# Optimization experiments

Measured on AMD Instinct MI355X. Metric: run time of the kernel, lower is better.

## Reference

```python
import jax, jax.numpy as jnp
import numpy as np

N = 50000
E = 800000
F_IN = 128
DIM = 256
NUM_CLASSES = 10
NUM_GRAPHS = 256


def setup_inputs() -> dict:
    key = jax.random.key(0)
    ks = jax.random.split(key, 20)
    x = jax.random.normal(ks[0], (N, F_IN), dtype=jnp.float32)
    edge_index = jax.random.randint(ks[1], (2, E), 0, N, dtype=jnp.int32)
    batch = jnp.sort(jax.random.randint(ks[2], (N,), 0, NUM_GRAPHS, dtype=jnp.int32))
    edge_weight = jnp.ones((E,), dtype=jnp.float32)

    def lin(k, fan_in, fan_out, bias=True):
        bound = 1.0 / np.sqrt(fan_in)
        k1, k2 = jax.random.split(k)
        W = jax.random.uniform(k1, (fan_in, fan_out), minval=-bound, maxval=bound, dtype=jnp.float32)
        if bias:
            b = jax.random.uniform(k2, (fan_out,), minval=-bound, maxval=bound, dtype=jnp.float32)
            return W, b
        return W

    params = {}
    dims = [(F_IN, DIM)] + [(DIM, DIM)] * 4
    for i, (fi, fo) in enumerate(dims, start=1):
        Wr, br = lin(ks[2 + 3 * i], fi, fo, bias=True)
        Wroot = lin(ks[3 + 3 * i], fi, fo, bias=False)
        params[f"W{i}_rel"] = Wr
        params[f"b{i}_rel"] = br
        params[f"W{i}_root"] = Wroot
    Wfc1, bfc1 = lin(ks[18], DIM, DIM)
    Wfc2, bfc2 = lin(ks[19], DIM, NUM_CLASSES)
    return dict(x=x, edge_index=edge_index, batch=batch, edge_weight=edge_weight,
                **params, Wfc1=Wfc1, bfc1=bfc1, Wfc2=Wfc2, bfc2=bfc2)


def graph_conv(x, src, dst, ew, W_rel, b_rel, W_root):
    # message: x_j * edge_weight, aggregated by sum at destination nodes
    msg = x[src] * ew[:, None]                                  # [E, F]
    agg = jax.ops.segment_sum(msg, dst, num_segments=N)          # [N, F]
    return agg @ W_rel + b_rel + x @ W_root


def reference(x, edge_index, batch, edge_weight,
              W1_rel, b1_rel, W1_root, W2_rel, b2_rel, W2_root,
              W3_rel, b3_rel, W3_root, W4_rel, b4_rel, W4_root,
              W5_rel, b5_rel, W5_root, Wfc1, bfc1, Wfc2, bfc2):
    src, dst = edge_index[0], edge_index[1]
    layers = [(W1_rel, b1_rel, W1_root), (W2_rel, b2_rel, W2_root),
              (W3_rel, b3_rel, W3_root), (W4_rel, b4_rel, W4_root),
              (W5_rel, b5_rel, W5_root)]
    h = x
    for Wr, br, Wroot in layers:
        h = jax.nn.relu(graph_conv(h, src, dst, edge_weight, Wr, br, Wroot))
    pooled = jax.ops.segment_sum(h, batch, num_segments=NUM_GRAPHS)  # [G, DIM]
    h = jax.nn.relu(pooled @ Wfc1 + bfc1)
    # dropout is identity in eval mode
    logits = h @ Wfc2 + bfc2
    return jax.nn.log_softmax(logits, axis=-1)
```

## Files before the change

### kernel.cpp

```cpp
#include <hip/hip_runtime.h>
#include <hip/hip_bf16.h>

#define N_NODES 50000
#define N_EDGES 800000
#define F_IN 128
#define DIM 256
#define NUM_CLASSES 10
#define NUM_GRAPHS 256
#define NBKT ((N_NODES + 255) / 256)
#define BCAP 8192
#define NRT ((N_NODES + 127) / 128)

typedef short bf16x8 __attribute__((ext_vector_type(8)));
typedef float f32x4 __attribute__((ext_vector_type(4)));

__device__ __forceinline__ float bf2f(unsigned short u) {
    union { unsigned int u; float f; } c;
    c.u = ((unsigned int)u) << 16;
    return c.f;
}
__device__ __forceinline__ unsigned short f2bf(float f) {
    union { float f; unsigned int u; } c;
    c.f = f;
    unsigned int r = (c.u + 0x7fffu + ((c.u >> 16) & 1u)) >> 16;
    return (unsigned short)r;
}
__device__ __forceinline__ float u2f(unsigned int u) {
    union { unsigned int u; float f; } c;
    c.u = u;
    return c.f;
}
__device__ __forceinline__ unsigned int f2u(float f) {
    union { float f; unsigned int u; } c;
    c.f = f;
    return c.u;
}

__device__ __forceinline__ void gload16(const unsigned short* g, unsigned short* l) {
    __builtin_amdgcn_global_load_lds(
        (const __attribute__((address_space(1))) unsigned int*)(g),
        (__attribute__((address_space(3))) unsigned int*)(l), 16, 0, 0);
}


__global__ void bucket_hist(const int* __restrict__ dst, int* __restrict__ bcnt, int E) {
    __shared__ int c[NBKT];
    int t = threadIdx.x;
    for (int i = t; i < NBKT; i += 256) c[i] = 0;
    __syncthreads();
    int ebase = blockIdx.x * 4096 + t;
#pragma unroll
    for (int i = 0; i < 16; ++i) {
        int e = ebase + i * 256;
        if (e < E) atomicAdd(&c[dst[e] >> 8], 1);
    }
    __syncthreads();
    for (int i = t; i < NBKT; i += 256)
        if (c[i]) atomicAdd(&bcnt[i], c[i]);
}

__global__ void scan_bkt(const int* __restrict__ bcnt, int* __restrict__ bbase,
                         int* __restrict__ gbase) {
    __shared__ int sd[256];
    int t = threadIdx.x;
    int v = (t < NBKT) ? bcnt[t] : 0;
    sd[t] = v;
    __syncthreads();
    for (int off = 1; off < 256; off <<= 1) {
        int u = (t >= off) ? sd[t - off] : 0;
        __syncthreads();
        sd[t] += u;
        __syncthreads();
    }
    if (t < NBKT) {
        int ex = sd[t] - v;
        bbase[t] = ex;
        gbase[t] = ex;
    }
    if (t == NBKT - 1) bbase[NBKT] = sd[t];
}

__global__ __launch_bounds__(256) void bucket_scatter(
    const int* __restrict__ src, const int* __restrict__ dst, const float* __restrict__ ew,
    int* __restrict__ gbase, uint2* __restrict__ edata2, int E) {
    __shared__ int cnt[NBKT];
    __shared__ int base_s[NBKT];
    int t = threadIdx.x;
    int ebase = blockIdx.x * 4096 + t;
    for (int i = t; i < NBKT; i += 256) cnt[i] = 0;
    __syncthreads();
#pragma unroll
    for (int i = 0; i < 16; ++i) {
        int e = ebase + i * 256;
        if (e < E) atomicAdd(&cnt[dst[e] >> 8], 1);
    }
    __syncthreads();
    for (int i = t; i < NBKT; i += 256) {
        int c = cnt[i];
        base_s[i] = c ? atomicAdd(&gbase[i], c) : 0;
        cnt[i] = 0;
    }
    __syncthreads();
#pragma unroll
    for (int i = 0; i < 16; ++i) {
        int e = ebase + i * 256;
        if (e < E) {
            int d = dst[e];
            int bkt = d >> 8;
            int r = atomicAdd(&cnt[bkt], 1);
            edata2[base_s[bkt] + r] =
                make_uint2((unsigned)src[e] | ((unsigned)(d & 255) << 16), f2u(ew[e]));
        }
    }
}

__global__ __launch_bounds__(256) void bucket_sort(
    const int* __restrict__ bbase, const uint2* __restrict__ edata2, uint2* __restrict__ edata,
    int* __restrict__ offs) {
    __shared__ uint2 stage[BCAP];
    __shared__ int cnt[256];
    __shared__ int sd[256];
    int b = blockIdx.x, t = threadIdx.x;
    int lo = bbase[b];
    int hi = bbase[b + 1];
    int ce = hi - lo;
    cnt[t] = 0;
    __syncthreads();
    for (int i = t; i < ce; i += 256) {
        uint2 e = edata2[lo + i];
        atomicAdd(&cnt[(e.x >> 16) & 255], 1);
    }
    __syncthreads();
    int myc = cnt[t];
    sd[t] = myc;
    __syncthreads();
    for (int off = 1; off < 256; off <<= 1) {
        int u = (t >= off) ? sd[t - off] : 0;
        __syncthreads();
        sd[t] += u;
        __syncthreads();
    }
    int ex = sd[t] - myc;
    __syncthreads();
    sd[t] = ex;
    cnt[t] = 0;
    int node = b * 256 + t;
    if (node < N_NODES) offs[node] = lo + ex;
    if (node == N_NODES - 1) offs[N_NODES] = lo + ex + myc;
    __syncthreads();
    if (ce <= BCAP) {
        for (int i = t; i < ce; i += 256) {
            uint2 e = edata2[lo + i];
            int dl = (e.x >> 16) & 255;
            int r = atomicAdd(&cnt[dl], 1);
            stage[sd[dl] + r] = make_uint2(e.x & 0xFFFFu, e.y);
        }
        __syncthreads();
        for (int i = t; i < ce; i += 256) edata[lo + i] = stage[i];
    } else {
        for (int i = t; i < ce; i += 256) {
            uint2 e = edata2[lo + i];
            int dl = (e.x >> 16) & 255;
            int r = atomicAdd(&cnt[dl], 1);
            edata[lo + sd[dl] + r] = make_uint2(e.x & 0xFFFFu, e.y);
        }
    }
}


__global__ void conv_x(const float* __restrict__ x, unsigned short* __restrict__ xb, int n4) {
    int i = blockIdx.x * blockDim.x + threadIdx.x;
    if (i >= n4) return;
    float4 v = ((const float4*)x)[i];
    ushort4 o;
    o.x = f2bf(v.x); o.y = f2bf(v.y); o.z = f2bf(v.z); o.w = f2bf(v.w);
    ((ushort4*)xb)[i] = o;
}

__global__ void pack_w(const float* __restrict__ Wr, const float* __restrict__ Wo,
                       unsigned short* __restrict__ Bt, int K) {
    int idx = blockIdx.x * blockDim.x + threadIdx.x;
    int total = 2 * K * DIM;
    if (idx >= total) return;
    int k = idx / DIM, c = idx % DIM;
    float v = (k < K) ? Wr[k * DIM + c] : Wo[(k - K) * DIM + c];
    Bt[(size_t)c * (2 * K) + k] = f2bf(v);
}

__global__ void pack_w4(const float* __restrict__ W2r, const float* __restrict__ W2o,
                        const float* __restrict__ W3r, const float* __restrict__ W3o,
                        const float* __restrict__ W4r, const float* __restrict__ W4o,
                        const float* __restrict__ W5r, const float* __restrict__ W5o,
                        unsigned short* __restrict__ B2, unsigned short* __restrict__ B3,
                        unsigned short* __restrict__ B4, unsigned short* __restrict__ B5) {
    int idx = blockIdx.x * blockDim.x + threadIdx.x;
    int total = 2 * DIM * DIM;
    if (idx >= total) return;
    int L = blockIdx.y;
    const float* Wr = (L == 0) ? W2r : (L == 1) ? W3r : (L == 2) ? W4r : W5r;
    const float* Wo = (L == 0) ? W2o : (L == 1) ? W3o : (L == 2) ? W4o : W5o;
    unsigned short* Bt = (L == 0) ? B2 : (L == 1) ? B3 : (L == 2) ? B4 : B5;
    int k = idx / DIM, c = idx % DIM;
    float v = (k < DIM) ? Wr[k * DIM + c] : Wo[(k - DIM) * DIM + c];
    Bt[(size_t)c * (2 * DIM) + k] = f2bf(v);
}


template <int F>
__global__ void agg_bf16(const unsigned short* __restrict__ hsrc, const int* __restrict__ offs,
                         const uint2* __restrict__ edata, unsigned short* __restrict__ agg) {
    int node = blockIdx.x * (blockDim.x >> 6) + (threadIdx.x >> 6);
    if (node >= N_NODES) return;
    int lane = threadIdx.x & 63;
    int hf = lane >> 5;
    int sl = lane & 31;
    int s0 = offs[node], s1 = offs[node + 1];
    if (F == 256) {
        const unsigned short* hb = hsrc + sl * 8;
        float acc[8] = {0.f, 0.f, 0.f, 0.f, 0.f, 0.f, 0.f, 0.f};
        int p = s0;
        for (; p + 7 < s1; p += 8) {
            uint2 e0 = edata[p + hf];
            uint2 e1 = edata[p + 2 + hf];
            uint2 e2 = edata[p + 4 + hf];
            uint2 e3 = edata[p + 6 + hf];
            float w0 = u2f(e0.y), w1 = u2f(e1.y), w2 = u2f(e2.y), w3 = u2f(e3.y);
            uint4 r0 = *(const uint4*)(hb + (size_t)e0.x * 256);
            uint4 r1 = *(const uint4*)(hb + (size_t)e1.x * 256);
            uint4 r2 = *(const uint4*)(hb + (size_t)e2.x * 256);
            uint4 r3 = *(const uint4*)(hb + (size_t)e3.x * 256);
            acc[0] += w0 * bf2f((unsigned short)r0.x);
            acc[1] += w0 * bf2f((unsigned short)(r0.x >> 16));
            acc[2] += w0 * bf2f((unsigned short)r0.y);
            acc[3] += w0 * bf2f((unsigned short)(r0.y >> 16));
            acc[4] += w0 * bf2f((unsigned short)r0.z);
            acc[5] += w0 * bf2f((unsigned short)(r0.z >> 16));
            acc[6] += w0 * bf2f((unsigned short)r0.w);
            acc[7] += w0 * bf2f((unsigned short)(r0.w >> 16));
            acc[0] += w1 * bf2f((unsigned short)r1.x);
            acc[1] += w1 * bf2f((unsigned short)(r1.x >> 16));
            acc[2] += w1 * bf2f((unsigned short)r1.y);
            acc[3] += w1 * bf2f((unsigned short)(r1.y >> 16));
            acc[4] += w1 * bf2f((unsigned short)r1.z);
            acc[5] += w1 * bf2f((unsigned short)(r1.z >> 16));
            acc[6] += w1 * bf2f((unsigned short)r1.w);
            acc[7] += w1 * bf2f((unsigned short)(r1.w >> 16));
            acc[0] += w2 * bf2f((unsigned short)r2.x);
            acc[1] += w2 * bf2f((unsigned short)(r2.x >> 16));
            acc[2] += w2 * bf2f((unsigned short)r2.y);
            acc[3] += w2 * bf2f((unsigned short)(r2.y >> 16));
            acc[4] += w2 * bf2f((unsigned short)r2.z);
            acc[5] += w2 * bf2f((unsigned short)(r2.z >> 16));
            acc[6] += w2 * bf2f((unsigned short)r2.w);
            acc[7] += w2 * bf2f((unsigned short)(r2.w >> 16));
            acc[0] += w3 * bf2f((unsigned short)r3.x);
            acc[1] += w3 * bf2f((unsigned short)(r3.x >> 16));
            acc[2] += w3 * bf2f((unsigned short)r3.y);
            acc[3] += w3 * bf2f((unsigned short)(r3.y >> 16));
            acc[4] += w3 * bf2f((unsigned short)r3.z);
            acc[5] += w3 * bf2f((unsigned short)(r3.z >> 16));
            acc[6] += w3 * bf2f((unsigned short)r3.w);
            acc[7] += w3 * bf2f((unsigned short)(r3.w >> 16));
        }
        for (; p + 3 < s1; p += 4) {
            uint2 e0 = edata[p + hf];
            uint2 e1 = edata[p + 2 + hf];
            float w0 = u2f(e0.y), w1 = u2f(e1.y);
            uint4 r0 = *(const uint4*)(hb + (size_t)e0.x * 256);
            uint4 r1 = *(const uint4*)(hb + (size_t)e1.x * 256);
            acc[0] += w0 * bf2f((unsigned short)r0.x);
            acc[1] += w0 * bf2f((unsigned short)(r0.x >> 16));
            acc[2] += w0 * bf2f((unsigned short)r0.y);
            acc[3] += w0 * bf2f((unsigned short)(r0.y >> 16));
            acc[4] += w0 * bf2f((unsigned short)r0.z);
            acc[5] += w0 * bf2f((unsigned short)(r0.z >> 16));
            acc[6] += w0 * bf2f((unsigned short)r0.w);
            acc[7] += w0 * bf2f((unsigned short)(r0.w >> 16));
            acc[0] += w1 * bf2f((unsigned short)r1.x);
            acc[1] += w1 * bf2f((unsigned short)(r1.x >> 16));
            acc[2] += w1 * bf2f((unsigned short)r1.y);
            acc[3] += w1 * bf2f((unsigned short)(r1.y >> 16));
            acc[4] += w1 * bf2f((unsigned short)r1.z);
            acc[5] += w1 * bf2f((unsigned short)(r1.z >> 16));
            acc[6] += w1 * bf2f((unsigned short)r1.w);
            acc[7] += w1 * bf2f((unsigned short)(r1.w >> 16));
        }
        for (; p < s1; p += 2) {
            int pe = p + hf;
            bool v = pe < s1;
            uint2 e = edata[v ? pe : (s1 - 1)];
            float w = v ? u2f(e.y) : 0.f;
            uint4 r = *(const uint4*)(hb + (size_t)e.x * 256);
            acc[0] += w * bf2f((unsigned short)r.x);
            acc[1] += w * bf2f((unsigned short)(r.x >> 16));
            acc[2] += w * bf2f((unsigned short)r.y);
            acc[3] += w * bf2f((unsigned short)(r.y >> 16));
            acc[4] += w * bf2f((unsigned short)r.z);
            acc[5] += w * bf2f((unsigned short)(r.z >> 16));
            acc[6] += w * bf2f((unsigned short)r.w);
            acc[7] += w * bf2f((unsigned short)(r.w >> 16));
        }
#pragma unroll
        for (int i = 0; i < 8; ++i) acc[i] += __shfl_xor(acc[i], 32, 64);
        if (hf == 0) {
            uint4 o;
            o.x = (unsigned)f2bf(acc[0]) | ((unsigned)f2bf(acc[1]) << 16);
            o.y = (unsigned)f2bf(acc[2]) | ((unsigned)f2bf(acc[3]) << 16);
            o.z = (unsigned)f2bf(acc[4]) | ((unsigned)f2bf(acc[5]) << 16);
            o.w = (unsigned)f2bf(acc[6]) | ((unsigned)f2bf(acc[7]) << 16);
            *(uint4*)(agg + (size_t)node * 256 + sl * 8) = o;
        }
    } else {
        const unsigned short* hb = hsrc + sl * 4;
        float acc[4] = {0.f, 0.f, 0.f, 0.f};
        int p = s0;
        for (; p + 7 < s1; p += 8) {
            uint2 e0 = edata[p + hf];
            uint2 e1 = edata[p + 2 + hf];
            uint2 e2 = edata[p + 4 + hf];
            uint2 e3 = edata[p + 6 + hf];
            float w0 = u2f(e0.y), w1 = u2f(e1.y), w2 = u2f(e2.y), w3 = u2f(e3.y);
            uint2 r0 = *(const uint2*)(hb + (size_t)e0.x * 128);
            uint2 r1 = *(const uint2*)(hb + (size_t)e1.x * 128);
            uint2 r2 = *(const uint2*)(hb + (size_t)e2.x * 128);
            uint2 r3 = *(const uint2*)(hb + (size_t)e3.x * 128);
            acc[0] += w0 * bf2f((unsigned short)r0.x);
            acc[1] += w0 * bf2f((unsigned short)(r0.x >> 16));
            acc[2] += w0 * bf2f((unsigned short)r0.y);
            acc[3] += w0 * bf2f((unsigned short)(r0.y >> 16));
            acc[0] += w1 * bf2f((unsigned short)r1.x);
            acc[1] += w1 * bf2f((unsigned short)(r1.x >> 16));
            acc[2] += w1 * bf2f((unsigned short)r1.y);
            acc[3] += w1 * bf2f((unsigned short)(r1.y >> 16));
            acc[0] += w2 * bf2f((unsigned short)r2.x);
            acc[1] += w2 * bf2f((unsigned short)(r2.x >> 16));
            acc[2] += w2 * bf2f((unsigned short)r2.y);
            acc[3] += w2 * bf2f((unsigned short)(r2.y >> 16));
            acc[0] += w3 * bf2f((unsigned short)r3.x);
            acc[1] += w3 * bf2f((unsigned short)(r3.x >> 16));
            acc[2] += w3 * bf2f((unsigned short)r3.y);
            acc[3] += w3 * bf2f((unsigned short)(r3.y >> 16));
        }
        for (; p + 3 < s1; p += 4) {
            uint2 e0 = edata[p + hf];
            uint2 e1 = edata[p + 2 + hf];
            float w0 = u2f(e0.y), w1 = u2f(e1.y);
            uint2 r0 = *(const uint2*)(hb + (size_t)e0.x * 128);
            uint2 r1 = *(const uint2*)(hb + (size_t)e1.x * 128);
            acc[0] += w0 * bf2f((unsigned short)r0.x);
            acc[1] += w0 * bf2f((unsigned short)(r0.x >> 16));
            acc[2] += w0 * bf2f((unsigned short)r0.y);
            acc[3] += w0 * bf2f((unsigned short)(r0.y >> 16));
            acc[0] += w1 * bf2f((unsigned short)r1.x);
            acc[1] += w1 * bf2f((unsigned short)(r1.x >> 16));
            acc[2] += w1 * bf2f((unsigned short)r1.y);
            acc[3] += w1 * bf2f((unsigned short)(r1.y >> 16));
        }
        for (; p < s1; p += 2) {
            int pe = p + hf;
            bool v = pe < s1;
            uint2 e = edata[v ? pe : (s1 - 1)];
            float w = v ? u2f(e.y) : 0.f;
            uint2 r = *(const uint2*)(hb + (size_t)e.x * 128);
            acc[0] += w * bf2f((unsigned short)r.x);
            acc[1] += w * bf2f((unsigned short)(r.x >> 16));
            acc[2] += w * bf2f((unsigned short)r.y);
            acc[3] += w * bf2f((unsigned short)(r.y >> 16));
        }
#pragma unroll
        for (int i = 0; i < 4; ++i) acc[i] += __shfl_xor(acc[i], 32, 64);
        if (hf == 0) {
            uint2 o;
            o.x = (unsigned)f2bf(acc[0]) | ((unsigned)f2bf(acc[1]) << 16);
            o.y = (unsigned)f2bf(acc[2]) | ((unsigned)f2bf(acc[3]) << 16);
            *(uint2*)(agg + (size_t)node * 128 + sl * 4) = o;
        }
    }
}


template <int K>
__global__ __launch_bounds__(256) void gemm_mfma(
    const unsigned short* __restrict__ A1, const unsigned short* __restrict__ A2,
    const unsigned short* __restrict__ Bt, const float* __restrict__ bias,
    unsigned short* __restrict__ out) {
    __shared__ unsigned short As[128 * 64];
    __shared__ unsigned short Bs[128 * 64];
    const int bb = blockIdx.x;
    const int chunkid = bb >> 4, ii = bb & 15;
    const int row_t = chunkid * 8 + (ii & 7);
    const int col_t = ii >> 3;
    if (row_t >= NRT) return;
    const int row0 = row_t * 128, col0 = col_t * 128;
    const int t = threadIdx.x;
    const int lane = t & 63;
    const int w = t >> 6;
    const int wr = w >> 1, wc = w & 1;
    const int fr = lane & 15, fq = lane >> 4;

    const int srow = t >> 3;
    const int schunk = (t & 7) ^ (srow & 7);

    int arow_[4];
#pragma unroll
    for (int g = 0; g < 4; ++g) {
        int r = row0 + g * 32 + srow;
        if (r >= N_NODES) r = N_NODES - 1;
        arow_[g] = r;
    }

    f32x4 acc[4][4] = {};

    constexpr int NT = (2 * K) / 64;
    for (int kt = 0; kt < NT; ++kt) {
        const int kk = kt * 64;
        const unsigned short* Ap;
        int ka;
        if (kk < K) { Ap = A1; ka = kk; } else { Ap = A2; ka = kk - K; }
#pragma unroll
        for (int g = 0; g < 4; ++g) {
            gload16(Ap + (size_t)arow_[g] * K + ka + schunk * 8, As + g * 2048 + w * 512);
            gload16(Bt + (size_t)(col0 + g * 32 + srow) * (2 * K) + kk + schunk * 8,
                    Bs + g * 2048 + w * 512);
        }
        __syncthreads();
        bf16x8 a[2][4], b[2][4];
#pragma unroll
        for (int kh = 0; kh < 2; ++kh) {
#pragma unroll
            for (int m = 0; m < 4; ++m) {
                int row = wr * 64 + m * 16 + fr;
                a[kh][m] = *(const bf16x8*)(As + row * 64 + ((kh * 4 + fq) ^ (row & 7)) * 8);
            }
#pragma unroll
            for (int n = 0; n < 4; ++n) {
                int row = wc * 64 + n * 16 + fr;
                b[kh][n] = *(const bf16x8*)(Bs + row * 64 + ((kh * 4 + fq) ^ (row & 7)) * 8);
            }
        }
#pragma unroll
        for (int kh = 0; kh < 2; ++kh)
#pragma unroll
            for (int m = 0; m < 4; ++m)
#pragma unroll
                for (int n = 0; n < 4; ++n)
                    acc[m][n] = __builtin_amdgcn_mfma_f32_16x16x32_bf16(a[kh][m], b[kh][n],
                                                                        acc[m][n], 0, 0, 0);
        __syncthreads();
    }

#pragma unroll
    for (int n = 0; n < 4; ++n) {
        const int col = col0 + wc * 64 + n * 16 + fr;
        const float bv = bias[col];
#pragma unroll
        for (int m = 0; m < 4; ++m) {
            const int rbase = row0 + wr * 64 + m * 16 + fq * 4;
#pragma unroll
            for (int j = 0; j < 4; ++j) {
                const int r = rbase + j;
                if (r < N_NODES)
                    out[(size_t)r * DIM + col] = f2bf(fmaxf(acc[m][n][j] + bv, 0.f));
            }
        }
    }
}


__global__ void pool_head_kernel(const unsigned short* __restrict__ h,
                                 const int* __restrict__ batch,
                                 const float* __restrict__ Wfc1, const float* __restrict__ bfc1,
                                 const float* __restrict__ Wfc2, const float* __restrict__ bfc2,
                                 float* __restrict__ out) {
    __shared__ float4 sd[4][64];
    __shared__ float row[DIM];
    __shared__ float fc1[DIM];
    __shared__ float logits[NUM_CLASSES];
    __shared__ float red[2];
    int g = blockIdx.x, t = threadIdx.x;
    int wv = t >> 6, lane = t & 63;
    int lo = 0, hi = N_NODES;
    while (lo < hi) { int m = (lo + hi) >> 1; if (batch[m] < g) lo = m + 1; else hi = m; }
    int start = lo;
    lo = 0; hi = N_NODES;
    while (lo < hi) { int m = (lo + hi) >> 1; if (batch[m] < g + 1) lo = m + 1; else hi = m; }
    int end = lo;
    float4 acc = {0.f, 0.f, 0.f, 0.f};
    for (int i = start + wv; i < end; i += 4) {
        uint2 r = *(const uint2*)(h + (size_t)i * 256 + lane * 4);
        acc.x += bf2f((unsigned short)r.x);
        acc.y += bf2f((unsigned short)(r.x >> 16));
        acc.z += bf2f((unsigned short)r.y);
        acc.w += bf2f((unsigned short)(r.y >> 16));
    }
    sd[wv][lane] = acc;
    __syncthreads();
    if (wv == 0) {
        float4 a = sd[0][lane], b = sd[1][lane], c = sd[2][lane], d = sd[3][lane];
        float4 s;
        s.x = a.x + b.x + c.x + d.x;
        s.y = a.y + b.y + c.y + d.y;
        s.z = a.z + b.z + c.z + d.z;
        s.w = a.w + b.w + c.w + d.w;
        *(float4*)(&row[lane * 4]) = s;
    }
    __syncthreads();
    float a1 = bfc1[t];
    for (int k = 0; k < DIM; ++k) a1 += row[k] * Wfc1[k * DIM + t];
    fc1[t] = fmaxf(a1, 0.f);
    __syncthreads();
    if (t < NUM_CLASSES) {
        float a = bfc2[t];
        for (int k = 0; k < DIM; ++k) a += fc1[k] * Wfc2[k * NUM_CLASSES + t];
        logits[t] = a;
    }
    __syncthreads();
    if (t == 0) {
        float mx = -INFINITY;
        for (int c2 = 0; c2 < NUM_CLASSES; ++c2) mx = fmaxf(mx, logits[c2]);
        float s = 0.f;
        for (int c2 = 0; c2 < NUM_CLASSES; ++c2) s += expf(logits[c2] - mx);
        red[0] = mx;
        red[1] = logf(s);
    }
    __syncthreads();
    if (t < NUM_CLASSES) out[g * NUM_CLASSES + t] = logits[t] - red[0] - red[1];
}


extern "C" void kernel_launch(void* const* d_in, const int* in_sizes, int n_in,
                              void* d_out, int out_size, void* d_ws, size_t ws_size,
                              hipStream_t stream) {
    const float* x = (const float*)d_in[0];
    const int* ei = (const int*)d_in[1];
    const int* batch = (const int*)d_in[2];
    const float* ew = (const float*)d_in[3];
    const float *Wr[5], *br[5], *Wo[5];
    for (int i = 0; i < 5; ++i) {
        Wr[i] = (const float*)d_in[4 + 3 * i];
        br[i] = (const float*)d_in[5 + 3 * i];
        Wo[i] = (const float*)d_in[6 + 3 * i];
    }
    const float* Wfc1 = (const float*)d_in[19];
    const float* bfc1 = (const float*)d_in[20];
    const float* Wfc2 = (const float*)d_in[21];
    const float* bfc2 = (const float*)d_in[22];
    float* out = (float*)d_out;

    char* ws = (char*)d_ws;
    size_t off = 0;
    auto alloc = [&](size_t bytes) {
        void* p = ws + off;
        off += (bytes + 255) & ~(size_t)255;
        return p;
    };
    unsigned short* xb = (unsigned short*)alloc((size_t)N_NODES * F_IN * 2);
    unsigned short* h0 = (unsigned short*)alloc((size_t)N_NODES * DIM * 2);
    unsigned short* h1 = (unsigned short*)alloc((size_t)N_NODES * DIM * 2);
    unsigned short* aggb = (unsigned short*)alloc((size_t)N_NODES * DIM * 2);
    unsigned short* Bt[5];
    Bt[0] = (unsigned short*)alloc((size_t)2 * F_IN * DIM * 2);
    for (int i = 1; i < 5; ++i) Bt[i] = (unsigned short*)alloc((size_t)2 * DIM * DIM * 2);
    int* offs = (int*)alloc((N_NODES + 1) * 4);
    int* bcnt = (int*)alloc(NBKT * 4);
    int* bbase = (int*)alloc((NBKT + 1) * 4);
    int* gbase = (int*)alloc(NBKT * 4);
    uint2* edata = (uint2*)alloc((size_t)N_EDGES * 8);
    uint2* edata2 = (uint2*)alloc((size_t)N_EDGES * 8);

    const int* src = ei;
    const int* dstp = ei + N_EDGES;

    hipMemsetAsync(bcnt, 0, NBKT * 4, stream);
    bucket_hist<<<(N_EDGES + 4095) / 4096, 256, 0, stream>>>(dstp, bcnt, N_EDGES);
    scan_bkt<<<1, 256, 0, stream>>>(bcnt, bbase, gbase);
    bucket_scatter<<<(N_EDGES + 4095) / 4096, 256, 0, stream>>>(src, dstp, ew, gbase, edata2,
                                                                N_EDGES);
    bucket_sort<<<NBKT, 256, 0, stream>>>(bbase, edata2, edata, offs);

    conv_x<<<((N_NODES * F_IN / 4) + 255) / 256, 256, 0, stream>>>(x, xb, N_NODES * F_IN / 4);
    pack_w<<<(2 * F_IN * DIM + 255) / 256, 256, 0, stream>>>(Wr[0], Wo[0], Bt[0], F_IN);
    {
        dim3 pg((2 * DIM * DIM + 255) / 256, 4);
        pack_w4<<<pg, 256, 0, stream>>>(Wr[1], Wo[1], Wr[2], Wo[2], Wr[3], Wo[3], Wr[4], Wo[4],
                                        Bt[1], Bt[2], Bt[3], Bt[4]);
    }

    const int ggrid = ((NRT + 7) / 8) * 16;

    agg_bf16<128><<<(N_NODES + 3) / 4, 256, 0, stream>>>(xb, offs, edata, aggb);
    gemm_mfma<128><<<ggrid, 256, 0, stream>>>(aggb, xb, Bt[0], br[0], h0);

    const unsigned short* hp = h0;
    unsigned short* hn = h1;
    for (int L = 1; L < 5; ++L) {
        agg_bf16<256><<<(N_NODES + 3) / 4, 256, 0, stream>>>(hp, offs, edata, aggb);
        gemm_mfma<256><<<ggrid, 256, 0, stream>>>(aggb, hp, Bt[L], br[L], hn);
        unsigned short* t2 = (unsigned short*)hp;
        hp = hn;
        hn = t2;
    }

    pool_head_kernel<<<NUM_GRAPHS, 256, 0, stream>>>(hp, batch, Wfc1, bfc1, Wfc2, bfc2, out);
}
```

Baseline: 528.5 us.

## Halve GEMM row tile to 64 and stage output through LDS for vectorized stores

The MFMA GEMM row tile shrinks from 128 to 64, which doubles the number of blocks, cuts accumulator registers per thread and should improve occupancy on a GPU with many compute units. The epilogue now writes the bias+ReLU bf16 results into shared memory (reusing the B tile buffer) and then emits coalesced 16-byte row stores instead of scattered 2-byte stores. In exchange, each block reloads the B tile for half as many rows, and the epilogue adds an extra barrier.

```diff
diff --git a/kernel.cpp b/kernel.cpp
--- a/kernel.cpp
+++ b/kernel.cpp
@@ -9,7 +9,7 @@
 #define NUM_GRAPHS 256
 #define NBKT ((N_NODES + 255) / 256)
 #define BCAP 8192
-#define NRT ((N_NODES + 127) / 128)
+#define NRT64 ((N_NODES + 63) / 64)
 
 typedef short bf16x8 __attribute__((ext_vector_type(8)));
 typedef float f32x4 __attribute__((ext_vector_type(4)));
@@ -384,14 +384,14 @@
     const unsigned short* __restrict__ A1, const unsigned short* __restrict__ A2,
     const unsigned short* __restrict__ Bt, const float* __restrict__ bias,
     unsigned short* __restrict__ out) {
-    __shared__ unsigned short As[128 * 64];
+    __shared__ unsigned short As[64 * 64];
     __shared__ unsigned short Bs[128 * 64];
     const int bb = blockIdx.x;
     const int chunkid = bb >> 4, ii = bb & 15;
     const int row_t = chunkid * 8 + (ii & 7);
     const int col_t = ii >> 3;
-    if (row_t >= NRT) return;
-    const int row0 = row_t * 128, col0 = col_t * 128;
+    if (row_t >= NRT64) return;
+    const int row0 = row_t * 64, col0 = col_t * 128;
     const int t = threadIdx.x;
     const int lane = t & 63;
     const int w = t >> 6;
@@ -401,15 +401,15 @@
     const int srow = t >> 3;
     const int schunk = (t & 7) ^ (srow & 7);
 
-    int arow_[4];
-#pragma unroll
-    for (int g = 0; g < 4; ++g) {
+    int arow_[2];
+#pragma unroll
+    for (int g = 0; g < 2; ++g) {
         int r = row0 + g * 32 + srow;
         if (r >= N_NODES) r = N_NODES - 1;
         arow_[g] = r;
     }
 
-    f32x4 acc[4][4] = {};
+    f32x4 acc[2][4] = {};
 
     constexpr int NT = (2 * K) / 64;
     for (int kt = 0; kt < NT; ++kt) {
@@ -418,18 +418,19 @@
         int ka;
         if (kk < K) { Ap = A1; ka = kk; } else { Ap = A2; ka = kk - K; }
 #pragma unroll
-        for (int g = 0; g < 4; ++g) {
+        for (int g = 0; g < 2; ++g)
             gload16(Ap + (size_t)arow_[g] * K + ka + schunk * 8, As + g * 2048 + w * 512);
+#pragma unroll
+        for (int g = 0; g < 4; ++g)
             gload16(Bt + (size_t)(col0 + g * 32 + srow) * (2 * K) + kk + schunk * 8,
                     Bs + g * 2048 + w * 512);
-        }
         __syncthreads();
-        bf16x8 a[2][4], b[2][4];
+        bf16x8 a[2][2], b[2][4];
 #pragma unroll
         for (int kh = 0; kh < 2; ++kh) {
 #pragma unroll
-            for (int m = 0; m < 4; ++m) {
-                int row = wr * 64 + m * 16 + fr;
+            for (int m = 0; m < 2; ++m) {
+                int row = wr * 32 + m * 16 + fr;
                 a[kh][m] = *(const bf16x8*)(As + row * 64 + ((kh * 4 + fq) ^ (row & 7)) * 8);
             }
 #pragma unroll
@@ -441,7 +442,7 @@
 #pragma unroll
         for (int kh = 0; kh < 2; ++kh)
 #pragma unroll
-            for (int m = 0; m < 4; ++m)
+            for (int m = 0; m < 2; ++m)
 #pragma unroll
                 for (int n = 0; n < 4; ++n)
                     acc[m][n] = __builtin_amdgcn_mfma_f32_16x16x32_bf16(a[kh][m], b[kh][n],
@@ -449,20 +450,28 @@
         __syncthreads();
     }
 
+    unsigned short* cs = Bs;
 #pragma unroll
     for (int n = 0; n < 4; ++n) {
-        const int col = col0 + wc * 64 + n * 16 + fr;
-        const float bv = bias[col];
-#pragma unroll
-        for (int m = 0; m < 4; ++m) {
-            const int rbase = row0 + wr * 64 + m * 16 + fq * 4;
-#pragma unroll
-            for (int j = 0; j < 4; ++j) {
-                const int r = rbase + j;
-                if (r < N_NODES)
-                    out[(size_t)r * DIM + col] = f2bf(fmaxf(acc[m][n][j] + bv, 0.f));
-            }
-        }
+        const int col = wc * 64 + n * 16 + fr;
+        const float bv = bias[col0 + col];
+#pragma unroll
+        for (int m = 0; m < 2; ++m) {
+            const int rl = wr * 32 + m * 16 + fq * 4;
+#pragma unroll
+            for (int j = 0; j < 4; ++j)
+                cs[(rl + j) * 128 + col] = f2bf(fmaxf(acc[m][n][j] + bv, 0.f));
+        }
+    }
+    __syncthreads();
+#pragma unroll
+    for (int pass = 0; pass < 4; ++pass) {
+        int idx = pass * 256 + t;
+        int cr = idx >> 4;
+        int cc = (idx & 15) * 8;
+        int r = row0 + cr;
+        if (r < N_NODES)
+            *(uint4*)(out + (size_t)r * DIM + col0 + cc) = *(const uint4*)(cs + cr * 128 + cc);
     }
 }
 
@@ -586,7 +595,7 @@
                                         Bt[1], Bt[2], Bt[3], Bt[4]);
     }
 
-    const int ggrid = ((NRT + 7) / 8) * 16;
+    const int ggrid = ((NRT64 + 7) / 8) * 16;
 
     agg_bf16<128><<<(N_NODES + 3) / 4, 256, 0, stream>>>(xb, offs, edata, aggb);
     gemm_mfma<128><<<ggrid, 256, 0, stream>>>(aggb, xb, Bt[0], br[0], h0);
```

After: 447.2 us. 15.4% less time.
